# Optimization experiments

Hardware: AMD Instinct MI355X
Metric: run time of the kernel (lower is better)

## Reference

```python
import jax, jax.numpy as jnp
import numpy as np

NUM_EXPERTS = 8
TOP_K = 2
HIDDEN = 1024
INTER = 1408
B, S = 2, 1024


def setup_inputs() -> dict:
    key = jax.random.key(0)
    k1, k2, k3, k4, k5 = jax.random.split(key, 5)
    scale = 0.02  # keep activations well-scaled
    return {
        "hidden_states": jax.random.normal(k1, (B, S, HIDDEN), dtype=jnp.float32),
        "gate_w": jax.random.normal(k2, (HIDDEN, NUM_EXPERTS), dtype=jnp.float32) * scale,
        "w_gate": jax.random.normal(k3, (NUM_EXPERTS, HIDDEN, INTER), dtype=jnp.float32) * scale,
        "w_up": jax.random.normal(k4, (NUM_EXPERTS, HIDDEN, INTER), dtype=jnp.float32) * scale,
        "w_down": jax.random.normal(k5, (NUM_EXPERTS, INTER, HIDDEN), dtype=jnp.float32) * scale,
    }


def reference(hidden_states, gate_w, w_gate, w_up, w_down):
    b, s, h = hidden_states.shape
    x = hidden_states.reshape(-1, h)  # [T, H]
    # Router: softmax in fp32, top-k, renormalize over selected experts
    logits = x @ gate_w  # [T, E]
    probs = jax.nn.softmax(logits.astype(jnp.float32), axis=-1)
    rw, sel = jax.lax.top_k(probs, TOP_K)  # [T, K]
    rw = rw / jnp.sum(rw, axis=-1, keepdims=True)
    rw = rw.astype(x.dtype)
    # Per-(token, expert) combine weight; duplicates summed (matches torch mask sum)
    combine = jnp.sum(rw[:, :, None] * jax.nn.one_hot(sel, NUM_EXPERTS, dtype=x.dtype), axis=1)  # [T, E]
    out = jnp.zeros_like(x)
    for e in range(NUM_EXPERTS):  # fixed small structural loop over experts
        inter = jax.nn.silu(x @ w_gate[e]) * (x @ w_up[e])  # [T, I]
        out = out + (inter @ w_down[e]) * combine[:, e:e + 1]
    return out.reshape(b, s, h)
```

## Files before the change

### kernel.cpp

```cpp
#include <hip/hip_runtime.h>
#include <hip/hip_bf16.h>

#define T_TOKENS 2048
#define HID 1024
#define ISZ 1408
#define NEXP 8
#define RMAXROWS 4608
#define TILES_MAX 72

typedef __bf16 bf16x8 __attribute__((ext_vector_type(8)));
typedef __bf16 bf16x4 __attribute__((ext_vector_type(4)));
typedef float  f32x16 __attribute__((ext_vector_type(16)));

__device__ __forceinline__ void gload16(const void* g, void* l) {
    __builtin_amdgcn_global_load_lds(
        (const __attribute__((address_space(1))) void*)g,
        (__attribute__((address_space(3))) void*)l,
        16, 0, 0);
}

#define PIPE_BARRIER(N)                                              \
    asm volatile("s_waitcnt vmcnt(" #N ") lgkmcnt(0)" ::: "memory"); \
    __builtin_amdgcn_sched_barrier(0);                               \
    __builtin_amdgcn_s_barrier();                                    \
    __builtin_amdgcn_sched_barrier(0);

__device__ __forceinline__ int sgwIdx(int e, int h) {
    return e * 1032 + h + (h >> 7);
}

__global__ __launch_bounds__(256) void router_kernel(
    const float* __restrict__ x, const float* __restrict__ gw,
    int* __restrict__ sel, float* __restrict__ wt,
    __bf16* __restrict__ xb)
{
    __shared__ float sgw[NEXP * 1032 + 8];
    for (int i = threadIdx.x; i < HID * NEXP; i += 256) {
        int h = i >> 3, e = i & 7;
        sgw[sgwIdx(e, h)] = gw[i];
    }
    __syncthreads();

    const int wave = threadIdx.x >> 6;
    const int lane = threadIdx.x & 63;
    const int t = blockIdx.x * 4 + wave;
    const float* xr = x + (size_t)t * HID;

    {
        const int c0 = lane * 16;
        float4 v0 = *(const float4*)(xr + c0);
        float4 v1 = *(const float4*)(xr + c0 + 4);
        float4 v2 = *(const float4*)(xr + c0 + 8);
        float4 v3 = *(const float4*)(xr + c0 + 12);
        bf16x8 o0, o1;
        o0[0]=(__bf16)v0.x; o0[1]=(__bf16)v0.y; o0[2]=(__bf16)v0.z; o0[3]=(__bf16)v0.w;
        o0[4]=(__bf16)v1.x; o0[5]=(__bf16)v1.y; o0[6]=(__bf16)v1.z; o0[7]=(__bf16)v1.w;
        o1[0]=(__bf16)v2.x; o1[1]=(__bf16)v2.y; o1[2]=(__bf16)v2.z; o1[3]=(__bf16)v2.w;
        o1[4]=(__bf16)v3.x; o1[5]=(__bf16)v3.y; o1[6]=(__bf16)v3.z; o1[7]=(__bf16)v3.w;
        *(bf16x8*)(xb + (size_t)t * HID + c0) = o0;
        *(bf16x8*)(xb + (size_t)t * HID + c0 + 8) = o1;
    }
    if (blockIdx.x == 0 && threadIdx.x < 128) {
        bf16x8 z;
        #pragma unroll
        for (int j = 0; j < 8; ++j) z[j] = (__bf16)0.f;
        *(bf16x8*)(xb + (size_t)T_TOKENS * HID + threadIdx.x * 8) = z;
    }

    const int e = lane & 7;
    const int c = lane >> 3;
    float acc = 0.f;
    #pragma unroll
    for (int h = c * 128; h < c * 128 + 128; h += 4) {
        float4 xv = *(const float4*)(xr + h);
        float4 wv = *(const float4*)&sgw[sgwIdx(e, h)];
        acc += xv.x * wv.x + xv.y * wv.y + xv.z * wv.z + xv.w * wv.w;
    }
    acc += __shfl_xor(acc, 8);
    acc += __shfl_xor(acc, 16);
    acc += __shfl_xor(acc, 32);
    float m = acc;
    #pragma unroll
    for (int d = 1; d < 8; d <<= 1) m = fmaxf(m, __shfl_xor(m, d));
    float p = expf(acc - m);
    float s = p;
    #pragma unroll
    for (int d = 1; d < 8; d <<= 1) s += __shfl_xor(s, d);
    p /= s;
    float p1 = p; int e1 = e;
    #pragma unroll
    for (int d = 1; d < 8; d <<= 1) {
        float op = __shfl_xor(p1, d); int oe = __shfl_xor(e1, d);
        if (op > p1 || (op == p1 && oe < e1)) { p1 = op; e1 = oe; }
    }
    float pm = (e == e1) ? -1.0f : p;
    float p2 = pm; int e2 = e;
    #pragma unroll
    for (int d = 1; d < 8; d <<= 1) {
        float op = __shfl_xor(p2, d); int oe = __shfl_xor(e2, d);
        if (op > p2 || (op == p2 && oe < e2)) { p2 = op; e2 = oe; }
    }
    if (lane == 0) {
        float inv = 1.0f / (p1 + p2);
        sel[t * 2 + 0] = e1; sel[t * 2 + 1] = e2;
        wt[t * 2 + 0] = p1 * inv; wt[t * 2 + 1] = p2 * inv;
    }
}

__global__ __launch_bounds__(256) void scan_assign_kernel(
    int* __restrict__ tiles,
    const int* __restrict__ sel, const float* __restrict__ wt,
    int* __restrict__ rtok, float* __restrict__ rwt, int* __restrict__ tok2row)
{
    __shared__ int hist[NEXP];
    __shared__ int soff[NEXP];
    __shared__ int scur[NEXP];
    if (threadIdx.x < NEXP) { hist[threadIdx.x] = 0; scur[threadIdx.x] = 0; }
    __syncthreads();
    for (int t = threadIdx.x; t < T_TOKENS; t += 256) {
        atomicAdd(&hist[sel[t * 2 + 0]], 1);
        atomicAdd(&hist[sel[t * 2 + 1]], 1);
    }
    __syncthreads();
    if (threadIdx.x == 0) {
        int cur = 0, tix = 0;
        for (int e = 0; e < NEXP; ++e) {
            soff[e] = cur;
            int n64 = (hist[e] + 63) & ~63;
            for (int rt = 0; rt * 64 < n64; ++rt)
                tiles[tix++] = (e << 16) | (cur + rt * 64);
            cur += n64;
        }
        for (; tix < TILES_MAX; ++tix) tiles[tix] = -1;
    }
    __syncthreads();
    for (int t = threadIdx.x; t < T_TOKENS; t += 256) {
        #pragma unroll
        for (int k = 0; k < 2; ++k) {
            int e = sel[t * 2 + k];
            int pos = atomicAdd(&scur[e], 1);
            int row = soff[e] + pos;
            rtok[row] = t + 1;
            rwt[row] = wt[t * 2 + k];
            tok2row[t * 2 + k] = row;
        }
    }
}

__global__ __launch_bounds__(256) void tcvt_all_kernel(
    const float* __restrict__ wg, const float* __restrict__ wu, const float* __restrict__ wd,
    __bf16* __restrict__ wgT, __bf16* __restrict__ wuT, __bf16* __restrict__ wdT)
{
    const int z = blockIdx.z;
    const int e = z & 7;
    const float* in;
    __bf16* out;
    int R, C, rrA, ccA, rrB, ccB;
    if (z < 16) {
        R = HID; C = ISZ;
        rrA = rrB = blockIdx.y * 64;
        ccA = (2 * blockIdx.x) * 64; ccB = ccA + 64;
        in  = (z < 8 ? wg : wu)  + (size_t)e * R * C;
        out = (z < 8 ? wgT : wuT) + (size_t)e * R * C;
    } else {
        R = ISZ; C = HID;
        ccA = ccB = blockIdx.y * 64;
        rrA = (2 * blockIdx.x) * 64; rrB = rrA + 64;
        in  = wd  + (size_t)e * R * C;
        out = wdT + (size_t)e * R * C;
    }
    __shared__ __bf16 tb[2][64][70];
    const int tid = threadIdx.x;
    const int lr  = tid >> 4;
    const int lc4 = (tid & 15) * 4;

    auto loadcvt = [&](int buf, int rr, int cc) {
        #pragma unroll
        for (int p = 0; p < 4; ++p) {
            float4 v = *(const float4*)(in + (size_t)(rr + p * 16 + lr) * C + cc + lc4);
            bf16x4 w;
            w[0] = (__bf16)v.x; w[1] = (__bf16)v.y; w[2] = (__bf16)v.z; w[3] = (__bf16)v.w;
            *(bf16x4*)&tb[buf][p * 16 + lr][lc4] = w;
        }
    };
    auto storeT = [&](int buf, int rr, int cc) {
        #pragma unroll
        for (int q = 0; q < 2; ++q) {
            const int oc = (tid >> 3) + 32 * q;
            const int vs = (tid & 7) * 8;
            bf16x8 w;
            #pragma unroll
            for (int j = 0; j < 8; ++j) w[j] = tb[buf][vs + j][oc];
            *(bf16x8*)(out + (size_t)(cc + oc) * R + rr + vs) = w;
        }
    };

    loadcvt(0, rrA, ccA);
    __syncthreads();
    loadcvt(1, rrB, ccB);
    storeT(0, rrA, ccA);
    __syncthreads();
    storeT(1, rrB, ccB);
}

__global__ __launch_bounds__(256) void ffn1_kernel(
    const __bf16* __restrict__ xb, const int* __restrict__ rtok,
    const __bf16* __restrict__ wgT, const __bf16* __restrict__ wuT,
    const int* __restrict__ tiles, __bf16* __restrict__ inter)
{
    const int n  = blockIdx.x;
    const int nn = (n & 7) * 198 + (n >> 3);
    const int i0 = (nn / TILES_MAX) * 64;
    const int tv = tiles[nn % TILES_MAX];
    if (tv < 0) return;
    const int e = tv >> 16;
    const int rowbase = tv & 0xFFFF;

    __shared__ __align__(16) __bf16 sA[4][64][32];
    __shared__ __align__(16) __bf16 sG[4][64][32];
    __shared__ __align__(16) __bf16 sU[4][64][32];

    const int lane = threadIdx.x & 63;
    const int wid  = threadIdx.x >> 6;
    const int wr = wid >> 1, wc = wid & 1;
    const int l31 = lane & 31;
    const int kg  = lane >> 5;

    const int r16 = lane >> 2;
    const int cz  = (((lane & 3) ^ ((r16 >> 1) & 3)) * 8);
    const int rowA = rowbase + wid * 16 + r16;
    const int tokp = rtok[rowA];
    const int src  = tokp ? (tokp - 1) : T_TOKENS;
    const __bf16* A0 = xb + (size_t)src * HID + cz;
    const size_t wb = (size_t)e * ISZ * HID + (size_t)(i0 + wid * 16 + r16) * HID + cz;
    const __bf16* G0 = wgT + wb;
    const __bf16* U0 = wuT + wb;

    f32x16 accG, accU;
    #pragma unroll
    for (int r = 0; r < 16; ++r) { accG[r] = 0.f; accU[r] = 0.f; }

    auto stage = [&](int b, int k0) {
        gload16(A0 + k0, &sA[b][wid * 16][0]);
        gload16(G0 + k0, &sG[b][wid * 16][0]);
        gload16(U0 + k0, &sU[b][wid * 16][0]);
    };
    auto compute = [&](int b) {
        #pragma unroll
        for (int s = 0; s < 2; ++s) {
            const int ch = ((2 * s + kg) ^ ((l31 >> 1) & 3)) * 8;
            bf16x8 a_ = *(const bf16x8*)&sA[b][wr * 32 + l31][ch];
            bf16x8 g_ = *(const bf16x8*)&sG[b][wc * 32 + l31][ch];
            bf16x8 u_ = *(const bf16x8*)&sU[b][wc * 32 + l31][ch];
            __builtin_amdgcn_s_setprio(1);
            accG = __builtin_amdgcn_mfma_f32_32x32x16_bf16(a_, g_, accG, 0, 0, 0);
            accU = __builtin_amdgcn_mfma_f32_32x32x16_bf16(a_, u_, accU, 0, 0, 0);
            __builtin_amdgcn_s_setprio(0);
        }
    };

    const int nIter = HID / 32;
    stage(0, 0);
    stage(1, 32);
    stage(2, 64);
    PIPE_BARRIER(6)
    for (int i = 0; i < nIter; ++i) {
        int ks = (i + 3 < nIter) ? (i + 3) * 32 : 0;
        stage((i + 3) & 3, ks);
        compute(i & 3);
        PIPE_BARRIER(6)
    }

    const int base_row = rowbase + wr * 32;
    #pragma unroll
    for (int r = 0; r < 16; ++r) {
        float g = accG[r];
        float u = accU[r];
        float v = g / (1.0f + __expf(-g)) * u;
        int row = base_row + (r & 3) + 8 * (r >> 2) + 4 * kg;
        inter[(size_t)row * ISZ + i0 + wc * 32 + l31] = (__bf16)v;
    }
}

__global__ __launch_bounds__(256) void ffn2_kernel(
    const __bf16* __restrict__ inter, const __bf16* __restrict__ wdT,
    const float* __restrict__ rwt, const int* __restrict__ tiles,
    float* __restrict__ y)
{
    const int n  = blockIdx.x;
    const int nn = (n & 7) * 144 + (n >> 3);
    const int n0 = (nn / TILES_MAX) * 64;
    const int tv = tiles[nn % TILES_MAX];
    if (tv < 0) return;
    const int e = tv >> 16;
    const int rowbase = tv & 0xFFFF;

    __shared__ __align__(16) __bf16 sA[4][64][32];
    __shared__ __align__(16) __bf16 sB[4][64][32];

    const int lane = threadIdx.x & 63;
    const int wid  = threadIdx.x >> 6;
    const int wr = wid >> 1, wc = wid & 1;
    const int l31 = lane & 31;
    const int kg  = lane >> 5;

    const int r16 = lane >> 2;
    const int cz  = (((lane & 3) ^ ((r16 >> 1) & 3)) * 8);
    const __bf16* A0 = inter + (size_t)(rowbase + wid * 16 + r16) * ISZ + cz;
    const __bf16* B0 = wdT + (size_t)e * HID * ISZ + (size_t)(n0 + wid * 16 + r16) * ISZ + cz;

    f32x16 acc;
    #pragma unroll
    for (int r = 0; r < 16; ++r) acc[r] = 0.f;

    auto stage = [&](int b, int k0) {
        gload16(A0 + k0, &sA[b][wid * 16][0]);
        gload16(B0 + k0, &sB[b][wid * 16][0]);
    };
    auto compute = [&](int b) {
        #pragma unroll
        for (int s = 0; s < 2; ++s) {
            const int ch = ((2 * s + kg) ^ ((l31 >> 1) & 3)) * 8;
            bf16x8 a_ = *(const bf16x8*)&sA[b][wr * 32 + l31][ch];
            bf16x8 b_ = *(const bf16x8*)&sB[b][wc * 32 + l31][ch];
            __builtin_amdgcn_s_setprio(1);
            acc = __builtin_amdgcn_mfma_f32_32x32x16_bf16(a_, b_, acc, 0, 0, 0);
            __builtin_amdgcn_s_setprio(0);
        }
    };

    const int nIter = ISZ / 32;
    stage(0, 0);
    stage(1, 32);
    stage(2, 64);
    PIPE_BARRIER(4)
    for (int i = 0; i < nIter; ++i) {
        int ks = (i + 3 < nIter) ? (i + 3) * 32 : 0;
        stage((i + 3) & 3, ks);
        compute(i & 3);
        PIPE_BARRIER(4)
    }

    const int base_row = rowbase + wr * 32;
    const int col = n0 + wc * 32 + l31;
    #pragma unroll
    for (int r = 0; r < 16; ++r) {
        int row = base_row + (r & 3) + 8 * (r >> 2) + 4 * kg;
        y[(size_t)row * HID + col] = rwt[row] * acc[r];
    }
}

__global__ __launch_bounds__(256) void combine_kernel(
    const float* __restrict__ y, const int* __restrict__ tok2row, float* __restrict__ out)
{
    const int idx = blockIdx.x * 256 + threadIdx.x;
    const int t = idx >> 8;
    const int c = (idx & 255) * 4;
    const int r0 = tok2row[t * 2];
    const int r1 = tok2row[t * 2 + 1];
    float4 a = *(const float4*)(y + (size_t)r0 * HID + c);
    float4 b = *(const float4*)(y + (size_t)r1 * HID + c);
    float4 o = {a.x + b.x, a.y + b.y, a.z + b.z, a.w + b.w};
    *(float4*)(out + (size_t)t * HID + c) = o;
}

extern "C" void kernel_launch(void* const* d_in, const int* in_sizes, int n_in,
                              void* d_out, int out_size, void* d_ws, size_t ws_size,
                              hipStream_t stream) {
    const float* x  = (const float*)d_in[0];
    const float* gw = (const float*)d_in[1];
    const float* wg = (const float*)d_in[2];
    const float* wu = (const float*)d_in[3];
    const float* wd = (const float*)d_in[4];
    float* out = (float*)d_out;

    char* ws = (char*)d_ws;
    int*    tiles   = (int*)(ws + 64);
    int*    sel     = (int*)(ws + 1024);
    float*  wtp     = (float*)(ws + 17408);
    int*    rtok    = (int*)(ws + 33792);
    float*  rwt     = (float*)(ws + 52224);
    int*    tok2row = (int*)(ws + 70656);
    __bf16* xb      = (__bf16*)(ws + 87040);
    __bf16* inter   = (__bf16*)(ws + 4283648);
    __bf16* wgT     = (__bf16*)(ws + 17260032);
    __bf16* wuT     = (__bf16*)(ws + 40328704);
    __bf16* wdT     = (__bf16*)(ws + 63397376);
    float*  y       = (float*)wgT;

    hipMemsetAsync(ws, 0, 87040, stream);

    tcvt_all_kernel<<<dim3(ISZ / 128, HID / 64, 24), 256, 0, stream>>>(wg, wu, wd, wgT, wuT, wdT);

    router_kernel<<<T_TOKENS / 4, 256, 0, stream>>>(x, gw, sel, wtp, xb);
    scan_assign_kernel<<<1, 256, 0, stream>>>(tiles, sel, wtp, rtok, rwt, tok2row);

    ffn1_kernel<<<22 * TILES_MAX, 256, 0, stream>>>(xb, rtok, wgT, wuT, tiles, inter);
    ffn2_kernel<<<16 * TILES_MAX, 256, 0, stream>>>(inter, wdT, rwt, tiles, y);
    combine_kernel<<<(T_TOKENS * HID / 4) / 256, 256, 0, stream>>>(y, tok2row, out);
}
```

Baseline: 155.7 us.

## Fuse weight transpose with router and scatter FFN2 output via atomics

Merges the weight transpose/convert kernel and the router into one prep kernel. Each transpose block now handles four 64x64 tiles instead of two, and the router blocks are appended after them, which cuts a launch and lets the two jobs overlap. The combine kernel and the y intermediate buffer are removed: FFN2 now atomically adds its weighted results straight into the output, which is zeroed beforehand with a memset. This trades a full read/write of y plus one launch for atomic contention and a non-deterministic summation order.

```diff
diff --git a/kernel.cpp b/kernel.cpp
--- a/kernel.cpp
+++ b/kernel.cpp
@@ -29,21 +29,87 @@
     return e * 1032 + h + (h >> 7);
 }
 
-__global__ __launch_bounds__(256) void router_kernel(
+__global__ __launch_bounds__(256) void prep_kernel(
     const float* __restrict__ x, const float* __restrict__ gw,
-    int* __restrict__ sel, float* __restrict__ wt,
-    __bf16* __restrict__ xb)
+    int* __restrict__ sel, float* __restrict__ wt, __bf16* __restrict__ xb,
+    const float* __restrict__ wg, const float* __restrict__ wu, const float* __restrict__ wd,
+    __bf16* __restrict__ wgT, __bf16* __restrict__ wuT, __bf16* __restrict__ wdT)
 {
-    __shared__ float sgw[NEXP * 1032 + 8];
-    for (int i = threadIdx.x; i < HID * NEXP; i += 256) {
+    __shared__ __align__(16) char smem[4 * 64 * 70 * 2];
+    const int bid = blockIdx.x;
+    const int tid = threadIdx.x;
+
+    if (bid < 2112) {
+        auto tb = (__bf16 (*)[64][70])smem;
+        const int z   = bid / 88;
+        const int rem = bid % 88;
+        const int bx  = rem >> 2;
+        const int by  = rem & 3;
+        const int e   = z & 7;
+        const float* in;
+        __bf16* out;
+        int R, C;
+        int rr[4], cc[4];
+        if (z < 16) {
+            R = HID; C = ISZ;
+            in  = (z < 8 ? wg : wu)  + (size_t)e * R * C;
+            out = (z < 8 ? wgT : wuT) + (size_t)e * R * C;
+            #pragma unroll
+            for (int q = 0; q < 4; ++q) { rr[q] = by * 256 + q * 64; cc[q] = bx * 64; }
+        } else {
+            R = ISZ; C = HID;
+            in  = wd  + (size_t)e * R * C;
+            out = wdT + (size_t)e * R * C;
+            #pragma unroll
+            for (int q = 0; q < 4; ++q) { rr[q] = bx * 64; cc[q] = by * 256 + q * 64; }
+        }
+        const int lr  = tid >> 4;
+        const int lc4 = (tid & 15) * 4;
+
+        auto loadcvt = [&](int buf, int r0, int c0) {
+            #pragma unroll
+            for (int p = 0; p < 4; ++p) {
+                float4 v = *(const float4*)(in + (size_t)(r0 + p * 16 + lr) * C + c0 + lc4);
+                bf16x4 w;
+                w[0] = (__bf16)v.x; w[1] = (__bf16)v.y; w[2] = (__bf16)v.z; w[3] = (__bf16)v.w;
+                *(bf16x4*)&tb[buf][p * 16 + lr][lc4] = w;
+            }
+        };
+        auto storeT = [&](int buf, int r0, int c0) {
+            #pragma unroll
+            for (int q = 0; q < 2; ++q) {
+                const int oc = (tid >> 3) + 32 * q;
+                const int vs = (tid & 7) * 8;
+                bf16x8 w;
+                #pragma unroll
+                for (int j = 0; j < 8; ++j) w[j] = tb[buf][vs + j][oc];
+                *(bf16x8*)(out + (size_t)(c0 + oc) * R + r0 + vs) = w;
+            }
+        };
+
+        loadcvt(0, rr[0], cc[0]);
+        __syncthreads();
+        loadcvt(1, rr[1], cc[1]); storeT(0, rr[0], cc[0]);
+        __syncthreads();
+        loadcvt(2, rr[2], cc[2]); storeT(1, rr[1], cc[1]);
+        __syncthreads();
+        loadcvt(3, rr[3], cc[3]); storeT(2, rr[2], cc[2]);
+        __syncthreads();
+        storeT(3, rr[3], cc[3]);
+        return;
+    }
+
+    float* sgw = (float*)smem;
+    for (int i = tid; i < HID * NEXP; i += 256) {
         int h = i >> 3, e = i & 7;
         sgw[sgwIdx(e, h)] = gw[i];
     }
     __syncthreads();
 
-    const int wave = threadIdx.x >> 6;
-    const int lane = threadIdx.x & 63;
-    const int t = blockIdx.x * 4 + wave;
+    const int rb   = bid - 2112;
+    const int wave = tid >> 6;
+    const int lane = tid & 63;
+    const int t = rb * 4 + wave;
     const float* xr = x + (size_t)t * HID;
 
     {
@@ -60,11 +126,11 @@
         *(bf16x8*)(xb + (size_t)t * HID + c0) = o0;
         *(bf16x8*)(xb + (size_t)t * HID + c0 + 8) = o1;
     }
-    if (blockIdx.x == 0 && threadIdx.x < 128) {
-        bf16x8 z;
+    if (rb == 0 && tid < 128) {
+        bf16x8 z8;
         #pragma unroll
-        for (int j = 0; j < 8; ++j) z[j] = (__bf16)0.f;
-        *(bf16x8*)(xb + (size_t)T_TOKENS * HID + threadIdx.x * 8) = z;
+        for (int j = 0; j < 8; ++j) z8[j] = (__bf16)0.f;
+        *(bf16x8*)(xb + (size_t)T_TOKENS * HID + tid * 8) = z8;
     }
 
     const int e = lane & 7;
@@ -110,7 +176,7 @@
 __global__ __launch_bounds__(256) void scan_assign_kernel(
     int* __restrict__ tiles,
     const int* __restrict__ sel, const float* __restrict__ wt,
-    int* __restrict__ rtok, float* __restrict__ rwt, int* __restrict__ tok2row)
+    int* __restrict__ rtok, float* __restrict__ rwt)
 {
     __shared__ int hist[NEXP];
     __shared__ int soff[NEXP];
@@ -142,65 +208,8 @@
             int row = soff[e] + pos;
             rtok[row] = t + 1;
             rwt[row] = wt[t * 2 + k];
-            tok2row[t * 2 + k] = row;
-        }
-    }
-}
-
-__global__ __launch_bounds__(256) void tcvt_all_kernel(
-    const float* __restrict__ wg, const float* __restrict__ wu, const float* __restrict__ wd,
-    __bf16* __restrict__ wgT, __bf16* __restrict__ wuT, __bf16* __restrict__ wdT)
-{
-    const int z = blockIdx.z;
-    const int e = z & 7;
-    const float* in;
-    __bf16* out;
-    int R, C, rrA, ccA, rrB, ccB;
-    if (z < 16) {
-        R = HID; C = ISZ;
-        rrA = rrB = blockIdx.y * 64;
-        ccA = (2 * blockIdx.x) * 64; ccB = ccA + 64;
-        in  = (z < 8 ? wg : wu)  + (size_t)e * R * C;
-        out = (z < 8 ? wgT : wuT) + (size_t)e * R * C;
-    } else {
-        R = ISZ; C = HID;
-        ccA = ccB = blockIdx.y * 64;
-        rrA = (2 * blockIdx.x) * 64; rrB = rrA + 64;
-        in  = wd  + (size_t)e * R * C;
-        out = wdT + (size_t)e * R * C;
-    }
-    __shared__ __bf16 tb[2][64][70];
-    const int tid = threadIdx.x;
-    const int lr  = tid >> 4;
-    const int lc4 = (tid & 15) * 4;
-
-    auto loadcvt = [&](int buf, int rr, int cc) {
-        #pragma unroll
-        for (int p = 0; p < 4; ++p) {
-            float4 v = *(const float4*)(in + (size_t)(rr + p * 16 + lr) * C + cc + lc4);
-            bf16x4 w;
-            w[0] = (__bf16)v.x; w[1] = (__bf16)v.y; w[2] = (__bf16)v.z; w[3] = (__bf16)v.w;
-            *(bf16x4*)&tb[buf][p * 16 + lr][lc4] = w;
-        }
-    };
-    auto storeT = [&](int buf, int rr, int cc) {
-        #pragma unroll
-        for (int q = 0; q < 2; ++q) {
-            const int oc = (tid >> 3) + 32 * q;
-            const int vs = (tid & 7) * 8;
-            bf16x8 w;
-            #pragma unroll
-            for (int j = 0; j < 8; ++j) w[j] = tb[buf][vs + j][oc];
-            *(bf16x8*)(out + (size_t)(cc + oc) * R + rr + vs) = w;
-        }
-    };
-
-    loadcvt(0, rrA, ccA);
-    __syncthreads();
-    loadcvt(1, rrB, ccB);
-    storeT(0, rrA, ccA);
-    __syncthreads();
-    storeT(1, rrB, ccB);
+        }
+    }
 }
 
 __global__ __launch_bounds__(256) void ffn1_kernel(
@@ -284,8 +293,8 @@
 
 __global__ __launch_bounds__(256) void ffn2_kernel(
     const __bf16* __restrict__ inter, const __bf16* __restrict__ wdT,
-    const float* __restrict__ rwt, const int* __restrict__ tiles,
-    float* __restrict__ y)
+    const float* __restrict__ rwt, const int* __restrict__ rtok,
+    const int* __restrict__ tiles, float* __restrict__ out)
 {
     const int n  = blockIdx.x;
     const int nn = (n & 7) * 144 + (n >> 3);
@@ -346,22 +355,10 @@
     #pragma unroll
     for (int r = 0; r < 16; ++r) {
         int row = base_row + (r & 3) + 8 * (r >> 2) + 4 * kg;
-        y[(size_t)row * HID + col] = rwt[row] * acc[r];
-    }
-}
-
-__global__ __launch_bounds__(256) void combine_kernel(
-    const float* __restrict__ y, const int* __restrict__ tok2row, float* __restrict__ out)
-{
-    const int idx = blockIdx.x * 256 + threadIdx.x;
-    const int t = idx >> 8;
-    const int c = (idx & 255) * 4;
-    const int r0 = tok2row[t * 2];
-    const int r1 = tok2row[t * 2 + 1];
-    float4 a = *(const float4*)(y + (size_t)r0 * HID + c);
-    float4 b = *(const float4*)(y + (size_t)r1 * HID + c);
-    float4 o = {a.x + b.x, a.y + b.y, a.z + b.z, a.w + b.w};
-    *(float4*)(out + (size_t)t * HID + c) = o;
+        int tp = rtok[row];
+        if (tp)
+            atomicAdd(&out[(size_t)(tp - 1) * HID + col], rwt[row] * acc[r]);
+    }
 }
 
 extern "C" void kernel_launch(void* const* d_in, const int* in_sizes, int n_in,
@@ -380,22 +377,18 @@
     float*  wtp     = (float*)(ws + 17408);
     int*    rtok    = (int*)(ws + 33792);
     float*  rwt     = (float*)(ws + 52224);
-    int*    tok2row = (int*)(ws + 70656);
     __bf16* xb      = (__bf16*)(ws + 87040);
     __bf16* inter   = (__bf16*)(ws + 4283648);
     __bf16* wgT     = (__bf16*)(ws + 17260032);
     __bf16* wuT     = (__bf16*)(ws + 40328704);
     __bf16* wdT     = (__bf16*)(ws + 63397376);
-    float*  y       = (float*)wgT;
 
     hipMemsetAsync(ws, 0, 87040, stream);
-
-    tcvt_all_kernel<<<dim3(ISZ / 128, HID / 64, 24), 256, 0, stream>>>(wg, wu, wd, wgT, wuT, wdT);
-
-    router_kernel<<<T_TOKENS / 4, 256, 0, stream>>>(x, gw, sel, wtp, xb);
-    scan_assign_kernel<<<1, 256, 0, stream>>>(tiles, sel, wtp, rtok, rwt, tok2row);
+    hipMemsetAsync(out, 0, (size_t)T_TOKENS * HID * 4, stream);
+
+    prep_kernel<<<2624, 256, 0, stream>>>(x, gw, sel, wtp, xb, wg, wu, wd, wgT, wuT, wdT);
+    scan_assign_kernel<<<1, 256, 0, stream>>>(tiles, sel, wtp, rtok, rwt);
 
     ffn1_kernel<<<22 * TILES_MAX, 256, 0, stream>>>(xb, rtok, wgT, wuT, tiles, inter);
-    ffn2_kernel<<<16 * TILES_MAX, 256, 0, stream>>>(inter, wdT, rwt, tiles, y);
-    combine_kernel<<<(T_TOKENS * HID / 4) / 256, 256, 0, stream>>>(y, tok2row, out);
-}
+    ffn2_kernel<<<16 * TILES_MAX, 256, 0, stream>>>(inter, wdT, rwt, rtok, tiles, out);
+}
```

Result: slower. 182.0 us (+16.9%).

## Use 128-row token tiles in ffn1 to double weight reuse per block

Applied to the files above, without the earlier changes.

Expert segments are now padded to multiples of 128 rows. ffn1 processes 128 token rows by 64 intermediate columns per block, so each warp issues four MFMAs per k-step and every gate/up weight tile loaded into LDS is reused across twice as many tokens. ffn2 keeps 64-row tiles through a separate tile list. The aim is to halve weight-tile traffic in ffn1 and raise MFMA density per barrier. The cost is more padding rows, which means wasted compute, larger workspace offsets, and higher register and LDS use per block.

```diff
diff --git a/kernel.cpp b/kernel.cpp
--- a/kernel.cpp
+++ b/kernel.cpp
@@ -5,8 +5,9 @@
 #define HID 1024
 #define ISZ 1408
 #define NEXP 8
-#define RMAXROWS 4608
-#define TILES_MAX 72
+#define RMAXROWS 5120
+#define T64_MAX 80
+#define T128_MAX 40
 
 typedef __bf16 bf16x8 __attribute__((ext_vector_type(8)));
 typedef __bf16 bf16x4 __attribute__((ext_vector_type(4)));
@@ -108,7 +109,7 @@
 }
 
 __global__ __launch_bounds__(256) void scan_assign_kernel(
-    int* __restrict__ tiles,
+    int* __restrict__ tiles64, int* __restrict__ tiles128,
     const int* __restrict__ sel, const float* __restrict__ wt,
     int* __restrict__ rtok, float* __restrict__ rwt, int* __restrict__ tok2row)
 {
@@ -123,15 +124,18 @@
     }
     __syncthreads();
     if (threadIdx.x == 0) {
-        int cur = 0, tix = 0;
+        int cur = 0, t64 = 0, t128 = 0;
         for (int e = 0; e < NEXP; ++e) {
             soff[e] = cur;
-            int n64 = (hist[e] + 63) & ~63;
-            for (int rt = 0; rt * 64 < n64; ++rt)
-                tiles[tix++] = (e << 16) | (cur + rt * 64);
-            cur += n64;
-        }
-        for (; tix < TILES_MAX; ++tix) tiles[tix] = -1;
+            int n128 = (hist[e] + 127) & ~127;
+            for (int rt = 0; rt * 64 < n128; ++rt)
+                tiles64[t64++] = (e << 16) | (cur + rt * 64);
+            for (int rt = 0; rt * 128 < n128; ++rt)
+                tiles128[t128++] = (e << 16) | (cur + rt * 128);
+            cur += n128;
+        }
+        for (; t64 < T64_MAX; ++t64) tiles64[t64] = -1;
+        for (; t128 < T128_MAX; ++t128) tiles128[t128] = -1;
     }
     __syncthreads();
     for (int t = threadIdx.x; t < T_TOKENS; t += 256) {
@@ -206,17 +210,17 @@
 __global__ __launch_bounds__(256) void ffn1_kernel(
     const __bf16* __restrict__ xb, const int* __restrict__ rtok,
     const __bf16* __restrict__ wgT, const __bf16* __restrict__ wuT,
-    const int* __restrict__ tiles, __bf16* __restrict__ inter)
+    const int* __restrict__ tiles128, __bf16* __restrict__ inter)
 {
     const int n  = blockIdx.x;
-    const int nn = (n & 7) * 198 + (n >> 3);
-    const int i0 = (nn / TILES_MAX) * 64;
-    const int tv = tiles[nn % TILES_MAX];
+    const int nn = (n & 7) * 110 + (n >> 3);
+    const int i0 = (nn / T128_MAX) * 64;
+    const int tv = tiles128[nn % T128_MAX];
     if (tv < 0) return;
     const int e = tv >> 16;
     const int rowbase = tv & 0xFFFF;
 
-    __shared__ __align__(16) __bf16 sA[4][64][32];
+    __shared__ __align__(16) __bf16 sA[4][128][32];
     __shared__ __align__(16) __bf16 sG[4][64][32];
     __shared__ __align__(16) __bf16 sU[4][64][32];
 
@@ -228,20 +232,25 @@
 
     const int r16 = lane >> 2;
     const int cz  = (((lane & 3) ^ ((r16 >> 1) & 3)) * 8);
-    const int rowA = rowbase + wid * 16 + r16;
-    const int tokp = rtok[rowA];
-    const int src  = tokp ? (tokp - 1) : T_TOKENS;
-    const __bf16* A0 = xb + (size_t)src * HID + cz;
+    const int rowA0 = rowbase + wid * 32 + r16;
+    const int rowA1 = rowA0 + 16;
+    const int tp0 = rtok[rowA0];
+    const int tp1 = rtok[rowA1];
+    const __bf16* A0 = xb + (size_t)(tp0 ? (tp0 - 1) : T_TOKENS) * HID + cz;
+    const __bf16* A1 = xb + (size_t)(tp1 ? (tp1 - 1) : T_TOKENS) * HID + cz;
     const size_t wb = (size_t)e * ISZ * HID + (size_t)(i0 + wid * 16 + r16) * HID + cz;
     const __bf16* G0 = wgT + wb;
     const __bf16* U0 = wuT + wb;
 
-    f32x16 accG, accU;
-    #pragma unroll
-    for (int r = 0; r < 16; ++r) { accG[r] = 0.f; accU[r] = 0.f; }
+    f32x16 accG[2], accU[2];
+    #pragma unroll
+    for (int m = 0; m < 2; ++m)
+        #pragma unroll
+        for (int r = 0; r < 16; ++r) { accG[m][r] = 0.f; accU[m][r] = 0.f; }
 
     auto stage = [&](int b, int k0) {
-        gload16(A0 + k0, &sA[b][wid * 16][0]);
+        gload16(A0 + k0, &sA[b][wid * 32][0]);
+        gload16(A1 + k0, &sA[b][wid * 32 + 16][0]);
         gload16(G0 + k0, &sG[b][wid * 16][0]);
         gload16(U0 + k0, &sU[b][wid * 16][0]);
     };
@@ -249,12 +258,15 @@
         #pragma unroll
         for (int s = 0; s < 2; ++s) {
             const int ch = ((2 * s + kg) ^ ((l31 >> 1) & 3)) * 8;
-            bf16x8 a_ = *(const bf16x8*)&sA[b][wr * 32 + l31][ch];
+            bf16x8 a0 = *(const bf16x8*)&sA[b][wr * 64 + l31][ch];
+            bf16x8 a1 = *(const bf16x8*)&sA[b][wr * 64 + 32 + l31][ch];
             bf16x8 g_ = *(const bf16x8*)&sG[b][wc * 32 + l31][ch];
             bf16x8 u_ = *(const bf16x8*)&sU[b][wc * 32 + l31][ch];
             __builtin_amdgcn_s_setprio(1);
-            accG = __builtin_amdgcn_mfma_f32_32x32x16_bf16(a_, g_, accG, 0, 0, 0);
-            accU = __builtin_amdgcn_mfma_f32_32x32x16_bf16(a_, u_, accU, 0, 0, 0);
+            accG[0] = __builtin_amdgcn_mfma_f32_32x32x16_bf16(a0, g_, accG[0], 0, 0, 0);
+            accG[1] = __builtin_amdgcn_mfma_f32_32x32x16_bf16(a1, g_, accG[1], 0, 0, 0);
+            accU[0] = __builtin_amdgcn_mfma_f32_32x32x16_bf16(a0, u_, accU[0], 0, 0, 0);
+            accU[1] = __builtin_amdgcn_mfma_f32_32x32x16_bf16(a1, u_, accU[1], 0, 0, 0);
             __builtin_amdgcn_s_setprio(0);
         }
     };
@@ -263,34 +275,38 @@
     stage(0, 0);
     stage(1, 32);
     stage(2, 64);
-    PIPE_BARRIER(6)
+    PIPE_BARRIER(8)
     for (int i = 0; i < nIter; ++i) {
         int ks = (i + 3 < nIter) ? (i + 3) * 32 : 0;
         stage((i + 3) & 3, ks);
         compute(i & 3);
-        PIPE_BARRIER(6)
-    }
-
-    const int base_row = rowbase + wr * 32;
-    #pragma unroll
-    for (int r = 0; r < 16; ++r) {
-        float g = accG[r];
-        float u = accU[r];
-        float v = g / (1.0f + __expf(-g)) * u;
-        int row = base_row + (r & 3) + 8 * (r >> 2) + 4 * kg;
-        inter[(size_t)row * ISZ + i0 + wc * 32 + l31] = (__bf16)v;
+        PIPE_BARRIER(8)
+    }
+
+    #pragma unroll
+    for (int m = 0; m < 2; ++m) {
+        const int base_row = rowbase + wr * 64 + m * 32;
+        const int col = i0 + wc * 32 + l31;
+        #pragma unroll
+        for (int r = 0; r < 16; ++r) {
+            float g = accG[m][r];
+            float u = accU[m][r];
+            float v = g / (1.0f + __expf(-g)) * u;
+            int row = base_row + (r & 3) + 8 * (r >> 2) + 4 * kg;
+            inter[(size_t)row * ISZ + col] = (__bf16)v;
+        }
     }
 }
 
 __global__ __launch_bounds__(256) void ffn2_kernel(
     const __bf16* __restrict__ inter, const __bf16* __restrict__ wdT,
-    const float* __restrict__ rwt, const int* __restrict__ tiles,
+    const float* __restrict__ rwt, const int* __restrict__ tiles64,
     float* __restrict__ y)
 {
     const int n  = blockIdx.x;
-    const int nn = (n & 7) * 144 + (n >> 3);
-    const int n0 = (nn / TILES_MAX) * 64;
-    const int tv = tiles[nn % TILES_MAX];
+    const int nn = (n & 7) * 160 + (n >> 3);
+    const int n0 = (nn / T64_MAX) * 64;
+    const int tv = tiles64[nn % T64_MAX];
     if (tv < 0) return;
     const int e = tv >> 16;
     const int rowbase = tv & 0xFFFF;
@@ -375,27 +391,28 @@
     float* out = (float*)d_out;
 
     char* ws = (char*)d_ws;
-    int*    tiles   = (int*)(ws + 64);
-    int*    sel     = (int*)(ws + 1024);
-    float*  wtp     = (float*)(ws + 17408);
-    int*    rtok    = (int*)(ws + 33792);
-    float*  rwt     = (float*)(ws + 52224);
-    int*    tok2row = (int*)(ws + 70656);
-    __bf16* xb      = (__bf16*)(ws + 87040);
-    __bf16* inter   = (__bf16*)(ws + 4283648);
-    __bf16* wgT     = (__bf16*)(ws + 17260032);
-    __bf16* wuT     = (__bf16*)(ws + 40328704);
-    __bf16* wdT     = (__bf16*)(ws + 63397376);
-    float*  y       = (float*)wgT;
-
-    hipMemsetAsync(ws, 0, 87040, stream);
+    int*    tiles64  = (int*)(ws + 64);
+    int*    tiles128 = (int*)(ws + 384);
+    int*    sel      = (int*)(ws + 1024);
+    float*  wtp      = (float*)(ws + 17408);
+    int*    rtok     = (int*)(ws + 33792);
+    float*  rwt      = (float*)(ws + 54272);
+    int*    tok2row  = (int*)(ws + 74752);
+    __bf16* xb       = (__bf16*)(ws + 91136);
+    __bf16* inter    = (__bf16*)(ws + 4287488);
+    __bf16* wgT      = (__bf16*)(ws + 18705408);
+    __bf16* wuT      = (__bf16*)(ws + 41774080);
+    __bf16* wdT      = (__bf16*)(ws + 64842752);
+    float*  y        = (float*)wgT;
+
+    hipMemsetAsync(ws, 0, 91136, stream);
 
     tcvt_all_kernel<<<dim3(ISZ / 128, HID / 64, 24), 256, 0, stream>>>(wg, wu, wd, wgT, wuT, wdT);
 
     router_kernel<<<T_TOKENS / 4, 256, 0, stream>>>(x, gw, sel, wtp, xb);
-    scan_assign_kernel<<<1, 256, 0, stream>>>(tiles, sel, wtp, rtok, rwt, tok2row);
-
-    ffn1_kernel<<<22 * TILES_MAX, 256, 0, stream>>>(xb, rtok, wgT, wuT, tiles, inter);
-    ffn2_kernel<<<16 * TILES_MAX, 256, 0, stream>>>(inter, wdT, rwt, tiles, y);
+    scan_assign_kernel<<<1, 256, 0, stream>>>(tiles64, tiles128, sel, wtp, rtok, rwt, tok2row);
+
+    ffn1_kernel<<<22 * T128_MAX, 256, 0, stream>>>(xb, rtok, wgT, wuT, tiles128, inter);
+    ffn2_kernel<<<16 * T64_MAX, 256, 0, stream>>>(inter, wdT, rwt, tiles64, y);
     combine_kernel<<<(T_TOKENS * HID / 4) / 256, 256, 0, stream>>>(y, tok2row, out);
 }
```

New measurement: 163.9 us. 5.3% more time.

## Fuse weight transpose with router and widen ffn2 N-tile to 128

Applied to the files above, without the earlier changes.

Merges the weight transpose/convert kernel and the router kernel into one launch that dispatches on block index. The router now computes all 8 logits per lane straight from global gate weights with a full-wave reduction, replacing the shared-memory staging. The ffn2 kernel doubles its output tile width to 128 columns, using two MFMA accumulators per wave so each A tile is reused twice, and halves the grid. This cuts a launch and A-operand traffic, at the cost of more registers and LDS per ffn2 block and fewer ffn2 blocks.

```diff
diff --git a/kernel.cpp b/kernel.cpp
--- a/kernel.cpp
+++ b/kernel.cpp
@@ -5,7 +5,6 @@
 #define HID 1024
 #define ISZ 1408
 #define NEXP 8
-#define RMAXROWS 4608
 #define TILES_MAX 72
 
 typedef __bf16 bf16x8 __attribute__((ext_vector_type(8)));
@@ -25,33 +24,83 @@
     __builtin_amdgcn_s_barrier();                                    \
     __builtin_amdgcn_sched_barrier(0);
 
-__device__ __forceinline__ int sgwIdx(int e, int h) {
-    return e * 1032 + h + (h >> 7);
-}
-
-__global__ __launch_bounds__(256) void router_kernel(
+__global__ __launch_bounds__(256) void prep_kernel(
     const float* __restrict__ x, const float* __restrict__ gw,
-    int* __restrict__ sel, float* __restrict__ wt,
-    __bf16* __restrict__ xb)
+    int* __restrict__ sel, float* __restrict__ wt, __bf16* __restrict__ xb,
+    const float* __restrict__ wg, const float* __restrict__ wu, const float* __restrict__ wd,
+    __bf16* __restrict__ wgT, __bf16* __restrict__ wuT, __bf16* __restrict__ wdT)
 {
-    __shared__ float sgw[NEXP * 1032 + 8];
-    for (int i = threadIdx.x; i < HID * NEXP; i += 256) {
-        int h = i >> 3, e = i & 7;
-        sgw[sgwIdx(e, h)] = gw[i];
-    }
-    __syncthreads();
-
-    const int wave = threadIdx.x >> 6;
-    const int lane = threadIdx.x & 63;
-    const int t = blockIdx.x * 4 + wave;
+    __shared__ __bf16 tb[2][64][70];
+    const int bid = blockIdx.x;
+    const int tid = threadIdx.x;
+
+    if (bid < 4224) {
+        const int z   = bid / 176;
+        const int rem = bid % 176;
+        const int bx  = rem >> 4;
+        const int by  = rem & 15;
+        const int e   = z & 7;
+        const float* in;
+        __bf16* out;
+        int R, C, rrA, ccA, rrB, ccB;
+        if (z < 16) {
+            R = HID; C = ISZ;
+            rrA = rrB = by * 64;
+            ccA = bx * 128; ccB = ccA + 64;
+            in  = (z < 8 ? wg : wu)  + (size_t)e * R * C;
+            out = (z < 8 ? wgT : wuT) + (size_t)e * R * C;
+        } else {
+            R = ISZ; C = HID;
+            ccA = ccB = by * 64;
+            rrA = bx * 128; rrB = rrA + 64;
+            in  = wd  + (size_t)e * R * C;
+            out = wdT + (size_t)e * R * C;
+        }
+        const int lr  = tid >> 4;
+        const int lc4 = (tid & 15) * 4;
+
+        auto loadcvt = [&](int buf, int rr, int cc) {
+            #pragma unroll
+            for (int p = 0; p < 4; ++p) {
+                float4 v = *(const float4*)(in + (size_t)(rr + p * 16 + lr) * C + cc + lc4);
+                bf16x4 w;
+                w[0] = (__bf16)v.x; w[1] = (__bf16)v.y; w[2] = (__bf16)v.z; w[3] = (__bf16)v.w;
+                *(bf16x4*)&tb[buf][p * 16 + lr][lc4] = w;
+            }
+        };
+        auto storeT = [&](int buf, int rr, int cc) {
+            #pragma unroll
+            for (int q = 0; q < 2; ++q) {
+                const int oc = (tid >> 3) + 32 * q;
+                const int vs = (tid & 7) * 8;
+                bf16x8 w;
+                #pragma unroll
+                for (int j = 0; j < 8; ++j) w[j] = tb[buf][vs + j][oc];
+                *(bf16x8*)(out + (size_t)(cc + oc) * R + rr + vs) = w;
+            }
+        };
+
+        loadcvt(0, rrA, ccA);
+        __syncthreads();
+        loadcvt(1, rrB, ccB);
+        storeT(0, rrA, ccA);
+        __syncthreads();
+        storeT(1, rrB, ccB);
+        return;
+    }
+
+    const int rb   = bid - 4224;
+    const int wave = tid >> 6;
+    const int lane = tid & 63;
+    const int t = rb * 4 + wave;
     const float* xr = x + (size_t)t * HID;
 
+    const int c0 = lane * 16;
+    float4 v0 = *(const float4*)(xr + c0);
+    float4 v1 = *(const float4*)(xr + c0 + 4);
+    float4 v2 = *(const float4*)(xr + c0 + 8);
+    float4 v3 = *(const float4*)(xr + c0 + 12);
     {
-        const int c0 = lane * 16;
-        float4 v0 = *(const float4*)(xr + c0);
-        float4 v1 = *(const float4*)(xr + c0 + 4);
-        float4 v2 = *(const float4*)(xr + c0 + 8);
-        float4 v3 = *(const float4*)(xr + c0 + 12);
         bf16x8 o0, o1;
         o0[0]=(__bf16)v0.x; o0[1]=(__bf16)v0.y; o0[2]=(__bf16)v0.z; o0[3]=(__bf16)v0.w;
         o0[4]=(__bf16)v1.x; o0[5]=(__bf16)v1.y; o0[6]=(__bf16)v1.z; o0[7]=(__bf16)v1.w;
@@ -60,46 +109,46 @@
         *(bf16x8*)(xb + (size_t)t * HID + c0) = o0;
         *(bf16x8*)(xb + (size_t)t * HID + c0 + 8) = o1;
     }
-    if (blockIdx.x == 0 && threadIdx.x < 128) {
-        bf16x8 z;
-        #pragma unroll
-        for (int j = 0; j < 8; ++j) z[j] = (__bf16)0.f;
-        *(bf16x8*)(xb + (size_t)T_TOKENS * HID + threadIdx.x * 8) = z;
-    }
-
-    const int e = lane & 7;
-    const int c = lane >> 3;
-    float acc = 0.f;
-    #pragma unroll
-    for (int h = c * 128; h < c * 128 + 128; h += 4) {
-        float4 xv = *(const float4*)(xr + h);
-        float4 wv = *(const float4*)&sgw[sgwIdx(e, h)];
-        acc += xv.x * wv.x + xv.y * wv.y + xv.z * wv.z + xv.w * wv.w;
-    }
-    acc += __shfl_xor(acc, 8);
-    acc += __shfl_xor(acc, 16);
-    acc += __shfl_xor(acc, 32);
-    float m = acc;
-    #pragma unroll
-    for (int d = 1; d < 8; d <<= 1) m = fmaxf(m, __shfl_xor(m, d));
-    float p = expf(acc - m);
-    float s = p;
-    #pragma unroll
-    for (int d = 1; d < 8; d <<= 1) s += __shfl_xor(s, d);
-    p /= s;
-    float p1 = p; int e1 = e;
-    #pragma unroll
-    for (int d = 1; d < 8; d <<= 1) {
-        float op = __shfl_xor(p1, d); int oe = __shfl_xor(e1, d);
-        if (op > p1 || (op == p1 && oe < e1)) { p1 = op; e1 = oe; }
-    }
-    float pm = (e == e1) ? -1.0f : p;
-    float p2 = pm; int e2 = e;
-    #pragma unroll
-    for (int d = 1; d < 8; d <<= 1) {
-        float op = __shfl_xor(p2, d); int oe = __shfl_xor(e2, d);
-        if (op > p2 || (op == p2 && oe < e2)) { p2 = op; e2 = oe; }
-    }
+    if (rb == 0 && tid < 128) {
+        bf16x8 z8;
+        #pragma unroll
+        for (int j = 0; j < 8; ++j) z8[j] = (__bf16)0.f;
+        *(bf16x8*)(xb + (size_t)T_TOKENS * HID + tid * 8) = z8;
+    }
+
+    float le[8] = {0.f, 0.f, 0.f, 0.f, 0.f, 0.f, 0.f, 0.f};
+    float xv[16];
+    xv[0]=v0.x; xv[1]=v0.y; xv[2]=v0.z; xv[3]=v0.w;
+    xv[4]=v1.x; xv[5]=v1.y; xv[6]=v1.z; xv[7]=v1.w;
+    xv[8]=v2.x; xv[9]=v2.y; xv[10]=v2.z; xv[11]=v2.w;
+    xv[12]=v3.x; xv[13]=v3.y; xv[14]=v3.z; xv[15]=v3.w;
+    #pragma unroll
+    for (int j = 0; j < 16; ++j) {
+        const float* gr = gw + (size_t)(c0 + j) * NEXP;
+        float4 g0 = *(const float4*)gr;
+        float4 g1 = *(const float4*)(gr + 4);
+        le[0] += xv[j] * g0.x; le[1] += xv[j] * g0.y;
+        le[2] += xv[j] * g0.z; le[3] += xv[j] * g0.w;
+        le[4] += xv[j] * g1.x; le[5] += xv[j] * g1.y;
+        le[6] += xv[j] * g1.z; le[7] += xv[j] * g1.w;
+    }
+    #pragma unroll
+    for (int d = 1; d < 64; d <<= 1) {
+        #pragma unroll
+        for (int k = 0; k < 8; ++k) le[k] += __shfl_xor(le[k], d);
+    }
+    float m = le[0];
+    #pragma unroll
+    for (int k = 1; k < 8; ++k) m = fmaxf(m, le[k]);
+    float pe[8]; float s = 0.f;
+    #pragma unroll
+    for (int k = 0; k < 8; ++k) { pe[k] = expf(le[k] - m); s += pe[k]; }
+    int e1 = 0; float p1 = pe[0];
+    #pragma unroll
+    for (int k = 1; k < 8; ++k) if (pe[k] > p1) { p1 = pe[k]; e1 = k; }
+    int e2 = -1; float p2 = -1.f;
+    #pragma unroll
+    for (int k = 0; k < 8; ++k) if (k != e1 && pe[k] > p2) { p2 = pe[k]; e2 = k; }
     if (lane == 0) {
         float inv = 1.0f / (p1 + p2);
         sel[t * 2 + 0] = e1; sel[t * 2 + 1] = e2;
@@ -147,62 +196,6 @@
     }
 }
 
-__global__ __launch_bounds__(256) void tcvt_all_kernel(
-    const float* __restrict__ wg, const float* __restrict__ wu, const float* __restrict__ wd,
-    __bf16* __restrict__ wgT, __bf16* __restrict__ wuT, __bf16* __restrict__ wdT)
-{
-    const int z = blockIdx.z;
-    const int e = z & 7;
-    const float* in;
-    __bf16* out;
-    int R, C, rrA, ccA, rrB, ccB;
-    if (z < 16) {
-        R = HID; C = ISZ;
-        rrA = rrB = blockIdx.y * 64;
-        ccA = (2 * blockIdx.x) * 64; ccB = ccA + 64;
-        in  = (z < 8 ? wg : wu)  + (size_t)e * R * C;
-        out = (z < 8 ? wgT : wuT) + (size_t)e * R * C;
-    } else {
-        R = ISZ; C = HID;
-        ccA = ccB = blockIdx.y * 64;
-        rrA = (2 * blockIdx.x) * 64; rrB = rrA + 64;
-        in  = wd  + (size_t)e * R * C;
-        out = wdT + (size_t)e * R * C;
-    }
-    __shared__ __bf16 tb[2][64][70];
-    const int tid = threadIdx.x;
-    const int lr  = tid >> 4;
-    const int lc4 = (tid & 15) * 4;
-
-    auto loadcvt = [&](int buf, int rr, int cc) {
-        #pragma unroll
-        for (int p = 0; p < 4; ++p) {
-            float4 v = *(const float4*)(in + (size_t)(rr + p * 16 + lr) * C + cc + lc4);
-            bf16x4 w;
-            w[0] = (__bf16)v.x; w[1] = (__bf16)v.y; w[2] = (__bf16)v.z; w[3] = (__bf16)v.w;
-            *(bf16x4*)&tb[buf][p * 16 + lr][lc4] = w;
-        }
-    };
-    auto storeT = [&](int buf, int rr, int cc) {
-        #pragma unroll
-        for (int q = 0; q < 2; ++q) {
-            const int oc = (tid >> 3) + 32 * q;
-            const int vs = (tid & 7) * 8;
-            bf16x8 w;
-            #pragma unroll
-            for (int j = 0; j < 8; ++j) w[j] = tb[buf][vs + j][oc];
-            *(bf16x8*)(out + (size_t)(cc + oc) * R + rr + vs) = w;
-        }
-    };
-
-    loadcvt(0, rrA, ccA);
-    __syncthreads();
-    loadcvt(1, rrB, ccB);
-    storeT(0, rrA, ccA);
-    __syncthreads();
-    storeT(1, rrB, ccB);
-}
-
 __global__ __launch_bounds__(256) void ffn1_kernel(
     const __bf16* __restrict__ xb, const int* __restrict__ rtok,
     const __bf16* __restrict__ wgT, const __bf16* __restrict__ wuT,
@@ -288,15 +281,15 @@
     float* __restrict__ y)
 {
     const int n  = blockIdx.x;
-    const int nn = (n & 7) * 144 + (n >> 3);
-    const int n0 = (nn / TILES_MAX) * 64;
+    const int nn = (n & 7) * 72 + (n >> 3);
+    const int n0 = (nn / TILES_MAX) * 128;
     const int tv = tiles[nn % TILES_MAX];
     if (tv < 0) return;
     const int e = tv >> 16;
     const int rowbase = tv & 0xFFFF;
 
     __shared__ __align__(16) __bf16 sA[4][64][32];
-    __shared__ __align__(16) __bf16 sB[4][64][32];
+    __shared__ __align__(16) __bf16 sB[4][128][32];
 
     const int lane = threadIdx.x & 63;
     const int wid  = threadIdx.x >> 6;
@@ -307,24 +300,30 @@
     const int r16 = lane >> 2;
     const int cz  = (((lane & 3) ^ ((r16 >> 1) & 3)) * 8);
     const __bf16* A0 = inter + (size_t)(rowbase + wid * 16 + r16) * ISZ + cz;
-    const __bf16* B0 = wdT + (size_t)e * HID * ISZ + (size_t)(n0 + wid * 16 + r16) * ISZ + cz;
-
-    f32x16 acc;
-    #pragma unroll
-    for (int r = 0; r < 16; ++r) acc[r] = 0.f;
+    const __bf16* B0 = wdT + (size_t)e * HID * ISZ + (size_t)(n0 + wid * 32 + r16) * ISZ + cz;
+    const size_t rstepB = (size_t)16 * ISZ;
+
+    f32x16 acc[2];
+    #pragma unroll
+    for (int q = 0; q < 2; ++q)
+        #pragma unroll
+        for (int r = 0; r < 16; ++r) acc[q][r] = 0.f;
 
     auto stage = [&](int b, int k0) {
-        gload16(A0 + k0, &sA[b][wid * 16][0]);
-        gload16(B0 + k0, &sB[b][wid * 16][0]);
+        gload16(A0 + k0,          &sA[b][wid * 16][0]);
+        gload16(B0 + k0,          &sB[b][wid * 32][0]);
+        gload16(B0 + k0 + rstepB, &sB[b][wid * 32 + 16][0]);
     };
     auto compute = [&](int b) {
         #pragma unroll
         for (int s = 0; s < 2; ++s) {
             const int ch = ((2 * s + kg) ^ ((l31 >> 1) & 3)) * 8;
             bf16x8 a_ = *(const bf16x8*)&sA[b][wr * 32 + l31][ch];
-            bf16x8 b_ = *(const bf16x8*)&sB[b][wc * 32 + l31][ch];
+            bf16x8 b0 = *(const bf16x8*)&sB[b][wc * 64 + l31][ch];
+            bf16x8 b1 = *(const bf16x8*)&sB[b][wc * 64 + 32 + l31][ch];
             __builtin_amdgcn_s_setprio(1);
-            acc = __builtin_amdgcn_mfma_f32_32x32x16_bf16(a_, b_, acc, 0, 0, 0);
+            acc[0] = __builtin_amdgcn_mfma_f32_32x32x16_bf16(a_, b0, acc[0], 0, 0, 0);
+            acc[1] = __builtin_amdgcn_mfma_f32_32x32x16_bf16(a_, b1, acc[1], 0, 0, 0);
             __builtin_amdgcn_s_setprio(0);
         }
     };
@@ -333,20 +332,23 @@
     stage(0, 0);
     stage(1, 32);
     stage(2, 64);
-    PIPE_BARRIER(4)
+    PIPE_BARRIER(6)
     for (int i = 0; i < nIter; ++i) {
         int ks = (i + 3 < nIter) ? (i + 3) * 32 : 0;
         stage((i + 3) & 3, ks);
         compute(i & 3);
-        PIPE_BARRIER(4)
+        PIPE_BARRIER(6)
     }
 
     const int base_row = rowbase + wr * 32;
-    const int col = n0 + wc * 32 + l31;
-    #pragma unroll
-    for (int r = 0; r < 16; ++r) {
-        int row = base_row + (r & 3) + 8 * (r >> 2) + 4 * kg;
-        y[(size_t)row * HID + col] = rwt[row] * acc[r];
+    #pragma unroll
+    for (int q = 0; q < 2; ++q) {
+        const int col = n0 + wc * 64 + q * 32 + l31;
+        #pragma unroll
+        for (int r = 0; r < 16; ++r) {
+            int row = base_row + (r & 3) + 8 * (r >> 2) + 4 * kg;
+            y[(size_t)row * HID + col] = rwt[row] * acc[q][r];
+        }
     }
 }
 
@@ -390,12 +392,10 @@
 
     hipMemsetAsync(ws, 0, 87040, stream);
 
-    tcvt_all_kernel<<<dim3(ISZ / 128, HID / 64, 24), 256, 0, stream>>>(wg, wu, wd, wgT, wuT, wdT);
-
-    router_kernel<<<T_TOKENS / 4, 256, 0, stream>>>(x, gw, sel, wtp, xb);
+    prep_kernel<<<4736, 256, 0, stream>>>(x, gw, sel, wtp, xb, wg, wu, wd, wgT, wuT, wdT);
     scan_assign_kernel<<<1, 256, 0, stream>>>(tiles, sel, wtp, rtok, rwt, tok2row);
 
     ffn1_kernel<<<22 * TILES_MAX, 256, 0, stream>>>(xb, rtok, wgT, wuT, tiles, inter);
-    ffn2_kernel<<<16 * TILES_MAX, 256, 0, stream>>>(inter, wdT, rwt, tiles, y);
+    ffn2_kernel<<<8 * TILES_MAX, 256, 0, stream>>>(inter, wdT, rwt, tiles, y);
     combine_kernel<<<(T_TOKENS * HID / 4) / 256, 256, 0, stream>>>(y, tok2row, out);
 }
```

After: 154.9 us. Within noise of the previous version (-0.5%).
